# Kernel optimization log

Measured on AMD Instinct MI355X. Metric: run time of the kernel, lower is better.

## Reference

```python
import jax, jax.numpy as jnp
import numpy as np

NUM_EXECUTORS = 50
NUM_DAG_FEATURES = 3
EMB_DAG = 16
EMB_GLOB = 16
HIDDEN = [64, 64, 32]
B = 60000            # number of jobs (one per env in the batched rollout)
NODES_PER_JOB = 10
NODE_FEAT = 5


def _init_mlp(key, dims):
    ws, bs = [], []
    for i in range(len(dims) - 1):
        key, k = jax.random.split(key)
        scale = 1.0 / np.sqrt(dims[i])
        ws.append(jax.random.uniform(k, (dims[i], dims[i + 1]), jnp.float32, -scale, scale))
        bs.append(jnp.zeros((dims[i + 1],), jnp.float32))
    return ws, bs


def setup_inputs() -> dict:
    rng = np.random.default_rng(0)
    n_nodes = B * NODES_PER_JOB
    # dag_batch.ptr: job i owns nodes [i*NODES_PER_JOB, (i+1)*NODES_PER_JOB)
    ptr = np.arange(B + 1, dtype=np.int64) * NODES_PER_JOB
    job_indices = rng.permutation(B).astype(np.int64)
    # ragged action counts per job (exec_mask is a prefix mask of length num_exec_acts[i])
    num_exec_acts = rng.integers(1, NUM_EXECUTORS + 1, size=B).astype(np.int64)
    n_sel = num_exec_acts[job_indices]
    T = int(n_sel.sum())
    # per-ragged-row executor index: concat([arange(n) for n in n_sel]), vectorized
    starts = np.cumsum(n_sel) - n_sel
    exec_act_idx = (np.arange(T, dtype=np.int64) - np.repeat(starts, n_sel)).astype(np.int64)

    key = jax.random.key(0)
    k_x, k_hd, k_hg, k_mlp = jax.random.split(key, 4)
    x = jax.random.normal(k_x, (n_nodes, NODE_FEAT), jnp.float32)
    h_dag = jax.random.normal(k_hd, (B, EMB_DAG), jnp.float32)
    h_glob = jax.random.normal(k_hg, (B, EMB_GLOB), jnp.float32)

    in_dim = NUM_DAG_FEATURES + EMB_DAG + EMB_GLOB + 1  # 36
    ws, bs = _init_mlp(k_mlp, [in_dim] + HIDDEN + [1])

    return {
        "x": x,
        "h_dag": h_dag,
        "h_glob": h_glob,
        "ptr": jnp.asarray(ptr),
        "job_indices": jnp.asarray(job_indices),
        "num_exec_acts": jnp.asarray(num_exec_acts),
        "exec_act_idx": jnp.asarray(exec_act_idx),
        "W1": ws[0], "b1": bs[0],
        "W2": ws[1], "b2": bs[1],
        "W3": ws[2], "b3": bs[2],
        "W4": ws[3], "b4": bs[3],
    }


def reference(x, h_dag, h_glob, ptr, job_indices, num_exec_acts, exec_act_idx,
              W1, b1, W2, b2, W3, b3, W4, b4):
    T = exec_act_idx.shape[0]                       # total ragged action rows (static)
    J = job_indices.shape[0]
    # masked gather: dag features at each dag's start node, then select jobs
    x_dag = x[ptr[:-1], :NUM_DAG_FEATURES][job_indices]        # [J, 3]
    h_dag_sel = h_dag[job_indices]                              # [J, 16]
    x_h_dag = jnp.concatenate([x_dag, h_dag_sel], axis=1)       # [J, 19]
    # variable repeat_interleave -> gather by repeated row index
    n_sel = num_exec_acts[job_indices]
    rpt = jnp.repeat(jnp.arange(J), n_sel, total_repeat_length=T)
    x_h_rpt = x_h_dag[rpt]                                      # [T, 19]
    h_glob_rpt = h_glob[rpt]                                    # [T, 16]
    # exec action feature: k / num_executors for the k-th valid executor
    exec_actions = (exec_act_idx.astype(x.dtype) / NUM_EXECUTORS)[:, None]  # [T, 1]
    h = jnp.concatenate([x_h_rpt, h_glob_rpt, exec_actions], axis=1)        # [T, 36]
    h = jax.nn.relu(h @ W1 + b1)
    h = jax.nn.relu(h @ W2 + b2)
    h = jax.nn.relu(h @ W3 + b3)
    scores = (h @ W4 + b4).squeeze(-1)                          # [T]
    return scores
```

## Files before the change

### kernel.cpp

```cpp
#include <hip/hip_runtime.h>

#define TPB 256

using half8  = __attribute__((ext_vector_type(8))) _Float16;
using fp16x2 = __attribute__((ext_vector_type(2))) __fp16;
using f32x4  = __attribute__((ext_vector_type(4))) float;

static __device__ __forceinline__ unsigned short h2u(_Float16 h) {
    union { _Float16 h; unsigned short u; } v; v.h = h; return v.u;
}
static __device__ __forceinline__ unsigned pkrtz(float a, float b) {
    fp16x2 h = __builtin_amdgcn_cvt_pkrtz(a, b);
    return __builtin_bit_cast(unsigned, h);
}
template <int CTRL>
static __device__ __forceinline__ float dppmov(float x) {
    return __int_as_float(__builtin_amdgcn_mov_dpp(__float_as_int(x), CTRL, 0xF, 0xF, true));
}
#define DPP_SWAP 0xB1

__global__ __launch_bounds__(TPB) void k_prep(const float* __restrict__ x,
                                              const float* __restrict__ h_dag,
                                              const float* __restrict__ h_glob,
                                              const int* __restrict__ ptr,
                                              const int* __restrict__ job_indices,
                                              const int* __restrict__ num_exec_acts,
                                              int J, unsigned int* __restrict__ feat,
                                              int* __restrict__ bsum, int* __restrict__ jsv)
{
    __shared__ int sc[TPB];
    int j = blockIdx.x * TPB + threadIdx.x;
    int v = 0;
    if (j < J) {
        int ji   = job_indices[j];
        v        = num_exec_acts[ji];
        int node = ptr[ji];
        float f[40];
        f[0] = x[node * 5 + 0];
        f[1] = x[node * 5 + 1];
        f[2] = x[node * 5 + 2];
#pragma unroll
        for (int c = 0; c < 16; c++) f[3 + c]  = h_dag[ji * 16 + c];
#pragma unroll
        for (int c = 0; c < 16; c++) f[19 + c] = h_glob[j * 16 + c];
#pragma unroll
        for (int c = 35; c < 40; c++) f[c] = 0.0f;
        unsigned int w[20];
#pragma unroll
        for (int k = 0; k < 20; k++)
            w[k] = (unsigned)h2u((_Float16)f[2 * k]) | ((unsigned)h2u((_Float16)f[2 * k + 1]) << 16);
        uint4* dst = (uint4*)(feat + (size_t)j * 20);
#pragma unroll
        for (int qq = 0; qq < 5; qq++)
            dst[qq] = make_uint4(w[4 * qq], w[4 * qq + 1], w[4 * qq + 2], w[4 * qq + 3]);
    }
    sc[threadIdx.x] = v;
    __syncthreads();
    for (int d = 1; d < TPB; d <<= 1) {
        int add = (threadIdx.x >= d) ? sc[threadIdx.x - d] : 0;
        __syncthreads();
        sc[threadIdx.x] += add;
        __syncthreads();
    }
    if (j < J) jsv[j] = ((sc[threadIdx.x] - v) << 6) | v;
    if (threadIdx.x == TPB - 1) bsum[blockIdx.x] = sc[TPB - 1];
}

__global__ __launch_bounds__(TPB) void k_scan_wprep(const int* __restrict__ bsum, int nb,
                                                    int* __restrict__ boff,
                                                    const float* __restrict__ W1,
                                                    const float* __restrict__ b1,
                                                    const float* __restrict__ W2,
                                                    const float* __restrict__ b2,
                                                    const float* __restrict__ W3,
                                                    const float* __restrict__ b3,
                                                    const float* __restrict__ W4,
                                                    uint4* __restrict__ wfrag,
                                                    float4* __restrict__ bfrag)
{
    __shared__ int sc[TPB];
    int v = (threadIdx.x < nb) ? bsum[threadIdx.x] : 0;
    sc[threadIdx.x] = v;
    __syncthreads();
    for (int d = 1; d < TPB; d <<= 1) {
        int add = (threadIdx.x >= d) ? sc[threadIdx.x - d] : 0;
        __syncthreads();
        sc[threadIdx.x] += add;
        __syncthreads();
    }
    if (threadIdx.x < nb) boff[threadIdx.x] = sc[threadIdx.x] - v;

    if (threadIdx.x < 64) {
        int lane = threadIdx.x;
        int n = lane & 15, q = lane >> 4;
#pragma unroll
        for (int nt = 0; nt < 4; nt++) {
#pragma unroll
            for (int s = 0; s < 2; s++) {
                half8 w1f, w2f;
#pragma unroll
                for (int jj = 0; jj < 8; jj++) {
                    int ks = s * 32 + q * 8 + jj;
                    w1f[jj] = (ks < 36) ? (_Float16)W1[ks * 64 + nt * 16 + n] : (_Float16)0.0f;
                    w2f[jj] = (_Float16)W2[ks * 64 + nt * 16 + n];
                }
                wfrag[(nt * 2 + s) * 64 + lane]     = __builtin_bit_cast(uint4, w1f);
                wfrag[(8 + nt * 2 + s) * 64 + lane] = __builtin_bit_cast(uint4, w2f);
            }
        }
#pragma unroll
        for (int nt = 0; nt < 2; nt++) {
#pragma unroll
            for (int s = 0; s < 2; s++) {
                half8 w3f;
#pragma unroll
                for (int jj = 0; jj < 8; jj++) {
                    int ks = s * 32 + q * 8 + jj;
                    w3f[jj] = (_Float16)W3[ks * 32 + nt * 16 + n];
                }
                wfrag[(16 + nt * 2 + s) * 64 + lane] = __builtin_bit_cast(uint4, w3f);
            }
        }
        bfrag[0 * 64 + lane] = make_float4(b1[n], b1[16 + n], b1[32 + n], b1[48 + n]);
        bfrag[1 * 64 + lane] = make_float4(b2[n], b2[16 + n], b2[32 + n], b2[48 + n]);
        bfrag[2 * 64 + lane] = make_float4(b3[n], b3[16 + n], W4[n], W4[16 + n]);
    }
}

__global__ __launch_bounds__(TPB) void k_fill(const int* __restrict__ jsv,
                                              const int* __restrict__ boff,
                                              int J, int* __restrict__ rpt)
{
    int j = blockIdx.x * TPB + threadIdx.x;
    if (j >= J) return;
    int pv    = jsv[j];
    int v     = pv & 63;
    int start = boff[blockIdx.x] + (pv >> 6);
    for (int k = 0; k < v; k++) rpt[start + k] = j;
}

__global__ __launch_bounds__(TPB) void k_mlp_mfma(const unsigned int* __restrict__ feat,
                                                  const int* __restrict__ rpt,
                                                  const int* __restrict__ exec_act_idx,
                                                  const uint4* __restrict__ wfrag,
                                                  const float4* __restrict__ bfrag,
                                                  const float* __restrict__ b4,
                                                  float* __restrict__ out, int T, int numTiles)
{
    __shared__ __align__(16) char smem[4 * 8192];
    const int tid  = threadIdx.x;
    const int lane = tid & 63;
    const int wv   = tid >> 6;
    const int n    = lane & 15;
    const int q    = lane >> 4;
    char* slab0 = smem + wv * 8192;
    char* slab1 = slab0 + 4096;

    half8 bw1[4][2], bw2[4][2], bw3[2][2];
#pragma unroll
    for (int nt = 0; nt < 4; nt++)
#pragma unroll
        for (int s = 0; s < 2; s++) {
            bw1[nt][s] = __builtin_bit_cast(half8, wfrag[(nt * 2 + s) * 64 + lane]);
            bw2[nt][s] = __builtin_bit_cast(half8, wfrag[(8 + nt * 2 + s) * 64 + lane]);
        }
#pragma unroll
    for (int nt = 0; nt < 2; nt++)
#pragma unroll
        for (int s = 0; s < 2; s++)
            bw3[nt][s] = __builtin_bit_cast(half8, wfrag[(16 + nt * 2 + s) * 64 + lane]);

    float4 bf1 = bfrag[0 * 64 + lane];
    float4 bf2 = bfrag[1 * 64 + lane];
    float4 bf3 = bfrag[2 * 64 + lane];
    float bb1[4] = {bf1.x, bf1.y, bf1.z, bf1.w};
    float bb2[4] = {bf2.x, bf2.y, bf2.z, bf2.w};
    float bb3[2] = {bf3.x, bf3.y};
    const float w4a = bf3.z, w4b = bf3.w;
    const float b4v = b4[0];
    const int   swr = (n >> 1) & 7;
    const int   odd = n & 1;

    for (int tile = blockIdx.x; tile < numTiles; tile += gridDim.x) {
        const int rowbase = tile * 128 + wv * 32;

        half8 a1[2][2];
#pragma unroll
        for (int mt = 0; mt < 2; mt++) {
            int  rt    = rowbase + 16 * mt + n;
            bool valid = rt < T;
            int  j     = valid ? rpt[rt] : 0;
            const uint4* fsrc = (const uint4*)(feat + (size_t)j * 20);
            uint4 g0 = fsrc[q];
            a1[mt][0] = __builtin_bit_cast(half8, g0);
            uint4 g1 = make_uint4(0, 0, 0, 0);
            if (q == 0) {
                g1 = fsrc[4];
                float fe = valid ? (float)exec_act_idx[rt] * 0.02f : 0.0f;
                g1.y = (g1.y & 0xffffu) | ((unsigned)h2u((_Float16)fe) << 16);
            }
            a1[mt][1] = __builtin_bit_cast(half8, g1);
        }

#pragma unroll
        for (int mt = 0; mt < 2; mt++) {
            f32x4 acc[4];
#pragma unroll
            for (int nt = 0; nt < 4; nt++) { f32x4 c; c[0]=c[1]=c[2]=c[3]=bb1[nt]; acc[nt]=c; }
#pragma unroll
            for (int s = 0; s < 2; s++) {
#pragma unroll
                for (int nt = 0; nt < 4; nt++)
                    acc[nt] = __builtin_amdgcn_mfma_f32_16x16x32_f16(a1[mt][s], bw1[nt][s], acc[nt], 0, 0, 0);
            }
            unsigned* sl = (unsigned*)slab0;
#pragma unroll
            for (int nt = 0; nt < 4; nt++) {
                float v0 = fmaxf(acc[nt][0], 0.0f), v1 = fmaxf(acc[nt][1], 0.0f);
                float v2 = fmaxf(acc[nt][2], 0.0f), v3 = fmaxf(acc[nt][3], 0.0f);
                float t0 = dppmov<DPP_SWAP>(v0), t1 = dppmov<DPP_SWAP>(v1);
                float t2 = dppmov<DPP_SWAP>(v2), t3 = dppmov<DPP_SWAP>(v3);
                unsigned u0 = pkrtz(odd ? t2 : v0, odd ? v2 : t0);
                unsigned u1 = pkrtz(odd ? t3 : v1, odd ? v3 : t1);
                int rowA = 16 * mt + 4 * q + (odd ? 2 : 0);
                int c    = 2 * nt + (n >> 3);
                int a0   = (rowA * 8 + (c ^ ((rowA >> 1) & 7))) * 4 + ((n >> 1) & 3);
                sl[a0] = u0; sl[a0 + 32] = u1;
            }
        }

#pragma unroll
        for (int mt = 0; mt < 2; mt++) {
            const int M0 = 16 * mt;
            f32x4 acc[4];
#pragma unroll
            for (int nt = 0; nt < 4; nt++) { f32x4 c; c[0]=c[1]=c[2]=c[3]=bb2[nt]; acc[nt]=c; }
#pragma unroll
            for (int s = 0; s < 2; s++) {
                half8 a = *(const half8*)(slab0 + ((M0 + n) * 8 + ((s * 4 + q) ^ swr)) * 16);
#pragma unroll
                for (int nt = 0; nt < 4; nt++)
                    acc[nt] = __builtin_amdgcn_mfma_f32_16x16x32_f16(a, bw2[nt][s], acc[nt], 0, 0, 0);
            }
            unsigned* sl = (unsigned*)slab1;
#pragma unroll
            for (int nt = 0; nt < 4; nt++) {
                float v0 = fmaxf(acc[nt][0], 0.0f), v1 = fmaxf(acc[nt][1], 0.0f);
                float v2 = fmaxf(acc[nt][2], 0.0f), v3 = fmaxf(acc[nt][3], 0.0f);
                float t0 = dppmov<DPP_SWAP>(v0), t1 = dppmov<DPP_SWAP>(v1);
                float t2 = dppmov<DPP_SWAP>(v2), t3 = dppmov<DPP_SWAP>(v3);
                unsigned u0 = pkrtz(odd ? t2 : v0, odd ? v2 : t0);
                unsigned u1 = pkrtz(odd ? t3 : v1, odd ? v3 : t1);
                int rowA = M0 + 4 * q + (odd ? 2 : 0);
                int c    = 2 * nt + (n >> 3);
                int a0   = (rowA * 8 + (c ^ ((rowA >> 1) & 7))) * 4 + ((n >> 1) & 3);
                sl[a0] = u0; sl[a0 + 32] = u1;
            }
        }

#pragma unroll
        for (int mt = 0; mt < 2; mt++) {
            const int M0 = 16 * mt;
            f32x4 acc[2];
#pragma unroll
            for (int nt = 0; nt < 2; nt++) { f32x4 c; c[0]=c[1]=c[2]=c[3]=bb3[nt]; acc[nt]=c; }
#pragma unroll
            for (int s = 0; s < 2; s++) {
                half8 a = *(const half8*)(slab1 + ((M0 + n) * 8 + ((s * 4 + q) ^ swr)) * 16);
#pragma unroll
                for (int nt = 0; nt < 2; nt++)
                    acc[nt] = __builtin_amdgcn_mfma_f32_16x16x32_f16(a, bw3[nt][s], acc[nt], 0, 0, 0);
            }
            f32x4 red;
#pragma unroll
            for (int r = 0; r < 4; r++)
                red[r] = fmaxf(acc[0][r], 0.0f) * w4a + fmaxf(acc[1][r], 0.0f) * w4b;
#pragma unroll
            for (int r = 0; r < 4; r++) {
                red[r] += dppmov<0x121>(red[r]);
                red[r] += dppmov<0x122>(red[r]);
                red[r] += dppmov<0x124>(red[r]);
                red[r] += dppmov<0x128>(red[r]);
            }
            int t = rowbase + M0 + q * 4 + n;
            float val = (n == 0) ? red[0] : (n == 1) ? red[1] : (n == 2) ? red[2] : red[3];
            if (n < 4 && t < T) out[t] = val + b4v;
        }
    }
}

extern "C" void kernel_launch(void* const* d_in, const int* in_sizes, int n_in,
                              void* d_out, int out_size, void* d_ws, size_t ws_size,
                              hipStream_t stream)
{
    const float* x             = (const float*)d_in[0];
    const float* h_dag         = (const float*)d_in[1];
    const float* h_glob        = (const float*)d_in[2];
    const int*   ptr           = (const int*)d_in[3];
    const int*   job_indices   = (const int*)d_in[4];
    const int*   num_exec_acts = (const int*)d_in[5];
    const int*   exec_act_idx  = (const int*)d_in[6];
    const float* W1 = (const float*)d_in[7];
    const float* b1 = (const float*)d_in[8];
    const float* W2 = (const float*)d_in[9];
    const float* b2 = (const float*)d_in[10];
    const float* W3 = (const float*)d_in[11];
    const float* b3 = (const float*)d_in[12];
    const float* W4 = (const float*)d_in[13];
    const float* b4 = (const float*)d_in[14];
    float* out = (float*)d_out;

    int J  = in_sizes[4];
    int T  = in_sizes[6];
    int nb = (J + TPB - 1) / TPB;

    char* wsp = (char*)d_ws;
    int* rpt = (int*)wsp;
    wsp += (((size_t)T * 4) + 255) / 256 * 256;
    int* bsum = (int*)wsp;
    wsp += (((size_t)nb * 4) + 255) / 256 * 256;
    int* boff = (int*)wsp;
    wsp += (((size_t)nb * 4) + 255) / 256 * 256;
    int* jsv = (int*)wsp;
    wsp += (((size_t)J * 4) + 255) / 256 * 256;
    uint4* wfrag = (uint4*)wsp;
    wsp += 20 * 64 * 16;
    float4* bfrag = (float4*)wsp;
    wsp += 3 * 64 * 16;
    unsigned int* feat = (unsigned int*)wsp;

    k_prep<<<nb, TPB, 0, stream>>>(x, h_dag, h_glob, ptr, job_indices, num_exec_acts,
                                   J, feat, bsum, jsv);
    k_scan_wprep<<<1, TPB, 0, stream>>>(bsum, nb, boff, W1, b1, W2, b2, W3, b3, W4,
                                        wfrag, bfrag);
    k_fill<<<nb, TPB, 0, stream>>>(jsv, boff, J, rpt);

    int numTiles = (T + 127) / 128;
    int grid = numTiles < 1024 ? numTiles : 1024;
    k_mlp_mfma<<<grid, TPB, 0, stream>>>(feat, rpt, exec_act_idx, wfrag, bfrag, b4,
                                         out, T, numTiles);
}
```

Measured before the change: 181.0 us.

## Fuse prep, scan and fill into one decoupled-lookback kernel; share LDS slab

```diff
diff --git a/kernel.cpp b/kernel.cpp
--- a/kernel.cpp
+++ b/kernel.cpp
@@ -19,17 +19,31 @@
 }
 #define DPP_SWAP 0xB1
 
-__global__ __launch_bounds__(TPB) void k_prep(const float* __restrict__ x,
-                                              const float* __restrict__ h_dag,
-                                              const float* __restrict__ h_glob,
-                                              const int* __restrict__ ptr,
-                                              const int* __restrict__ job_indices,
-                                              const int* __restrict__ num_exec_acts,
-                                              int J, unsigned int* __restrict__ feat,
-                                              int* __restrict__ bsum, int* __restrict__ jsv)
+__global__ __launch_bounds__(TPB) void k_prep_fused(const float* __restrict__ x,
+                                                    const float* __restrict__ h_dag,
+                                                    const float* __restrict__ h_glob,
+                                                    const int* __restrict__ ptr,
+                                                    const int* __restrict__ job_indices,
+                                                    const int* __restrict__ num_exec_acts,
+                                                    const float* __restrict__ W1,
+                                                    const float* __restrict__ b1,
+                                                    const float* __restrict__ W2,
+                                                    const float* __restrict__ b2,
+                                                    const float* __restrict__ W3,
+                                                    const float* __restrict__ b3,
+                                                    const float* __restrict__ W4,
+                                                    int J,
+                                                    unsigned int* __restrict__ feat,
+                                                    unsigned long long* __restrict__ state,
+                                                    int* __restrict__ rpt,
+                                                    uint4* __restrict__ wfrag,
+                                                    float4* __restrict__ bfrag)
 {
     __shared__ int sc[TPB];
-    int j = blockIdx.x * TPB + threadIdx.x;
+    __shared__ int sPrefix;
+    const int tid = threadIdx.x;
+    const int b   = blockIdx.x;
+    int j = b * TPB + tid;
     int v = 0;
     if (j < J) {
         int ji   = job_indices[j];
@@ -54,89 +68,76 @@
         for (int qq = 0; qq < 5; qq++)
             dst[qq] = make_uint4(w[4 * qq], w[4 * qq + 1], w[4 * qq + 2], w[4 * qq + 3]);
     }
-    sc[threadIdx.x] = v;
+    sc[tid] = v;
     __syncthreads();
     for (int d = 1; d < TPB; d <<= 1) {
-        int add = (threadIdx.x >= d) ? sc[threadIdx.x - d] : 0;
+        int add = (tid >= d) ? sc[tid - d] : 0;
         __syncthreads();
-        sc[threadIdx.x] += add;
+        sc[tid] += add;
         __syncthreads();
     }
-    if (j < J) jsv[j] = ((sc[threadIdx.x] - v) << 6) | v;
-    if (threadIdx.x == TPB - 1) bsum[blockIdx.x] = sc[TPB - 1];
-}
-
-__global__ __launch_bounds__(TPB) void k_scan_wprep(const int* __restrict__ bsum, int nb,
-                                                    int* __restrict__ boff,
-                                                    const float* __restrict__ W1,
-                                                    const float* __restrict__ b1,
-                                                    const float* __restrict__ W2,
-                                                    const float* __restrict__ b2,
-                                                    const float* __restrict__ W3,
-                                                    const float* __restrict__ b3,
-                                                    const float* __restrict__ W4,
-                                                    uint4* __restrict__ wfrag,
-                                                    float4* __restrict__ bfrag)
-{
-    __shared__ int sc[TPB];
-    int v = (threadIdx.x < nb) ? bsum[threadIdx.x] : 0;
-    sc[threadIdx.x] = v;
+    if (tid == TPB - 1) {
+        int total = sc[TPB - 1];
+        long long pfx = 0;
+        if (b == 0) {
+            __threadfence();
+            atomicExch(state + 0, (2ULL << 32) | (unsigned)total);
+        } else {
+            __threadfence();
+            atomicExch(state + b, (1ULL << 32) | (unsigned)total);
+            int pb = b - 1;
+            while (pb >= 0) {
+                unsigned long long s = atomicAdd(state + pb, 0ULL);
+                unsigned stt = (unsigned)(s >> 32);
+                if (stt == 0) { __builtin_amdgcn_s_sleep(1); continue; }
+                pfx += (unsigned)(s & 0xffffffffu);
+                if (stt == 2) break;
+                pb--;
+            }
+            __threadfence();
+            atomicExch(state + b, (2ULL << 32) | (unsigned)((int)pfx + total));
+        }
+        sPrefix = (int)pfx;
+    }
     __syncthreads();
-    for (int d = 1; d < TPB; d <<= 1) {
-        int add = (threadIdx.x >= d) ? sc[threadIdx.x - d] : 0;
-        __syncthreads();
-        sc[threadIdx.x] += add;
-        __syncthreads();
-    }
-    if (threadIdx.x < nb) boff[threadIdx.x] = sc[threadIdx.x] - v;
-
-    if (threadIdx.x < 64) {
-        int lane = threadIdx.x;
-        int n = lane & 15, q = lane >> 4;
-#pragma unroll
-        for (int nt = 0; nt < 4; nt++) {
-#pragma unroll
-            for (int s = 0; s < 2; s++) {
-                half8 w1f, w2f;
+    int start = sPrefix + sc[tid] - v;
+    if (j < J) {
+        for (int k = 0; k < v; k++) rpt[start + k] = j;
+    }
+    if (b == 0) {
+        int lane = tid & 63;
+        int wvv  = tid >> 6;
+        int nn = lane & 15, qq = lane >> 4;
+        for (int f = wvv; f < 20; f += 4) {
+            half8 w;
+            if (f < 8) {
+                int nt = f >> 1, s = f & 1;
 #pragma unroll
                 for (int jj = 0; jj < 8; jj++) {
-                    int ks = s * 32 + q * 8 + jj;
-                    w1f[jj] = (ks < 36) ? (_Float16)W1[ks * 64 + nt * 16 + n] : (_Float16)0.0f;
-                    w2f[jj] = (_Float16)W2[ks * 64 + nt * 16 + n];
+                    int ks = s * 32 + qq * 8 + jj;
+                    w[jj] = (ks < 36) ? (_Float16)W1[ks * 64 + nt * 16 + nn] : (_Float16)0.0f;
                 }
-                wfrag[(nt * 2 + s) * 64 + lane]     = __builtin_bit_cast(uint4, w1f);
-                wfrag[(8 + nt * 2 + s) * 64 + lane] = __builtin_bit_cast(uint4, w2f);
-            }
-        }
-#pragma unroll
-        for (int nt = 0; nt < 2; nt++) {
-#pragma unroll
-            for (int s = 0; s < 2; s++) {
-                half8 w3f;
+            } else if (f < 16) {
+                int g = f - 8, nt = g >> 1, s = g & 1;
 #pragma unroll
                 for (int jj = 0; jj < 8; jj++) {
-                    int ks = s * 32 + q * 8 + jj;
-                    w3f[jj] = (_Float16)W3[ks * 32 + nt * 16 + n];
+                    int ks = s * 32 + qq * 8 + jj;
+                    w[jj] = (_Float16)W2[ks * 64 + nt * 16 + nn];
                 }
-                wfrag[(16 + nt * 2 + s) * 64 + lane] = __builtin_bit_cast(uint4, w3f);
-            }
-        }
-        bfrag[0 * 64 + lane] = make_float4(b1[n], b1[16 + n], b1[32 + n], b1[48 + n]);
-        bfrag[1 * 64 + lane] = make_float4(b2[n], b2[16 + n], b2[32 + n], b2[48 + n]);
-        bfrag[2 * 64 + lane] = make_float4(b3[n], b3[16 + n], W4[n], W4[16 + n]);
-    }
-}
-
-__global__ __launch_bounds__(TPB) void k_fill(const int* __restrict__ jsv,
-                                              const int* __restrict__ boff,
-                                              int J, int* __restrict__ rpt)
-{
-    int j = blockIdx.x * TPB + threadIdx.x;
-    if (j >= J) return;
-    int pv    = jsv[j];
-    int v     = pv & 63;
-    int start = boff[blockIdx.x] + (pv >> 6);
-    for (int k = 0; k < v; k++) rpt[start + k] = j;
+            } else {
+                int g = f - 16, nt = g >> 1, s = g & 1;
+#pragma unroll
+                for (int jj = 0; jj < 8; jj++) {
+                    int ks = s * 32 + qq * 8 + jj;
+                    w[jj] = (_Float16)W3[ks * 32 + nt * 16 + nn];
+                }
+            }
+            wfrag[f * 64 + lane] = __builtin_bit_cast(uint4, w);
+        }
+        if (wvv == 0) bfrag[0 * 64 + lane] = make_float4(b1[nn], b1[16 + nn], b1[32 + nn], b1[48 + nn]);
+        if (wvv == 1) bfrag[1 * 64 + lane] = make_float4(b2[nn], b2[16 + nn], b2[32 + nn], b2[48 + nn]);
+        if (wvv == 2) bfrag[2 * 64 + lane] = make_float4(b3[nn], b3[16 + nn], W4[nn], W4[16 + nn]);
+    }
 }
 
 __global__ __launch_bounds__(TPB) void k_mlp_mfma(const unsigned int* __restrict__ feat,
@@ -147,14 +148,13 @@
                                                   const float* __restrict__ b4,
                                                   float* __restrict__ out, int T, int numTiles)
 {
-    __shared__ __align__(16) char smem[4 * 8192];
+    __shared__ __align__(16) char smem[4 * 4096];
     const int tid  = threadIdx.x;
     const int lane = tid & 63;
     const int wv   = tid >> 6;
     const int n    = lane & 15;
     const int q    = lane >> 4;
-    char* slab0 = smem + wv * 8192;
-    char* slab1 = slab0 + 4096;
+    char* slab = smem + wv * 4096;
 
     half8 bw1[4][2], bw2[4][2], bw3[2][2];
 #pragma unroll
@@ -213,7 +213,7 @@
                 for (int nt = 0; nt < 4; nt++)
                     acc[nt] = __builtin_amdgcn_mfma_f32_16x16x32_f16(a1[mt][s], bw1[nt][s], acc[nt], 0, 0, 0);
             }
-            unsigned* sl = (unsigned*)slab0;
+            unsigned* sl = (unsigned*)slab;
 #pragma unroll
             for (int nt = 0; nt < 4; nt++) {
                 float v0 = fmaxf(acc[nt][0], 0.0f), v1 = fmaxf(acc[nt][1], 0.0f);
@@ -235,14 +235,15 @@
             f32x4 acc[4];
 #pragma unroll
             for (int nt = 0; nt < 4; nt++) { f32x4 c; c[0]=c[1]=c[2]=c[3]=bb2[nt]; acc[nt]=c; }
-#pragma unroll
-            for (int s = 0; s < 2; s++) {
-                half8 a = *(const half8*)(slab0 + ((M0 + n) * 8 + ((s * 4 + q) ^ swr)) * 16);
-#pragma unroll
-                for (int nt = 0; nt < 4; nt++)
-                    acc[nt] = __builtin_amdgcn_mfma_f32_16x16x32_f16(a, bw2[nt][s], acc[nt], 0, 0, 0);
-            }
-            unsigned* sl = (unsigned*)slab1;
+            half8 a0r = *(const half8*)(slab + ((M0 + n) * 8 + ((0 * 4 + q) ^ swr)) * 16);
+            half8 a1r = *(const half8*)(slab + ((M0 + n) * 8 + ((1 * 4 + q) ^ swr)) * 16);
+#pragma unroll
+            for (int nt = 0; nt < 4; nt++)
+                acc[nt] = __builtin_amdgcn_mfma_f32_16x16x32_f16(a0r, bw2[nt][0], acc[nt], 0, 0, 0);
+#pragma unroll
+            for (int nt = 0; nt < 4; nt++)
+                acc[nt] = __builtin_amdgcn_mfma_f32_16x16x32_f16(a1r, bw2[nt][1], acc[nt], 0, 0, 0);
+            unsigned* sl = (unsigned*)slab;
 #pragma unroll
             for (int nt = 0; nt < 4; nt++) {
                 float v0 = fmaxf(acc[nt][0], 0.0f), v1 = fmaxf(acc[nt][1], 0.0f);
@@ -266,7 +267,7 @@
             for (int nt = 0; nt < 2; nt++) { f32x4 c; c[0]=c[1]=c[2]=c[3]=bb3[nt]; acc[nt]=c; }
 #pragma unroll
             for (int s = 0; s < 2; s++) {
-                half8 a = *(const half8*)(slab1 + ((M0 + n) * 8 + ((s * 4 + q) ^ swr)) * 16);
+                half8 a = *(const half8*)(slab + ((M0 + n) * 8 + ((s * 4 + q) ^ swr)) * 16);
 #pragma unroll
                 for (int nt = 0; nt < 2; nt++)
                     acc[nt] = __builtin_amdgcn_mfma_f32_16x16x32_f16(a, bw3[nt][s], acc[nt], 0, 0, 0);
@@ -317,23 +318,18 @@
     char* wsp = (char*)d_ws;
     int* rpt = (int*)wsp;
     wsp += (((size_t)T * 4) + 255) / 256 * 256;
-    int* bsum = (int*)wsp;
-    wsp += (((size_t)nb * 4) + 255) / 256 * 256;
-    int* boff = (int*)wsp;
-    wsp += (((size_t)nb * 4) + 255) / 256 * 256;
-    int* jsv = (int*)wsp;
-    wsp += (((size_t)J * 4) + 255) / 256 * 256;
+    unsigned long long* state = (unsigned long long*)wsp;
+    wsp += (((size_t)nb * 8) + 255) / 256 * 256;
     uint4* wfrag = (uint4*)wsp;
     wsp += 20 * 64 * 16;
     float4* bfrag = (float4*)wsp;
     wsp += 3 * 64 * 16;
     unsigned int* feat = (unsigned int*)wsp;
 
-    k_prep<<<nb, TPB, 0, stream>>>(x, h_dag, h_glob, ptr, job_indices, num_exec_acts,
-                                   J, feat, bsum, jsv);
-    k_scan_wprep<<<1, TPB, 0, stream>>>(bsum, nb, boff, W1, b1, W2, b2, W3, b3, W4,
-                                        wfrag, bfrag);
-    k_fill<<<nb, TPB, 0, stream>>>(jsv, boff, J, rpt);
+    hipMemsetAsync(state, 0, (size_t)nb * 8, stream);
+    k_prep_fused<<<nb, TPB, 0, stream>>>(x, h_dag, h_glob, ptr, job_indices, num_exec_acts,
+                                         W1, b1, W2, b2, W3, b3, W4,
+                                         J, feat, state, rpt, wfrag, bfrag);
 
     int numTiles = (T + 127) / 128;
     int grid = numTiles < 1024 ? numTiles : 1024;
```

New measurement: 199.8 us. 1.1x slower.
